# Optimization experiments

Hardware: AMD Instinct MI355X
Metric: run time of the kernel (lower is better)

## Reference

```python
import jax, jax.numpy as jnp
import numpy as np

B, S, D = 2, 2048, 1024
H = 16
HD = D // H  # 64


def setup_inputs() -> dict:
    key = jax.random.key(0)
    ks = jax.random.split(key, 6)
    x = jax.random.normal(ks[0], (B, S, D), dtype=jnp.float32)
    sc = 1.0 / np.sqrt(D)
    Wq = jax.random.normal(ks[1], (D, D), dtype=jnp.float32) * sc
    Wk = jax.random.normal(ks[2], (D, D), dtype=jnp.float32) * sc
    Wv = jax.random.normal(ks[3], (D, D), dtype=jnp.float32) * sc
    Wo = jax.random.normal(ks[4], (D, D), dtype=jnp.float32) * sc
    bo = jax.random.normal(ks[5], (D,), dtype=jnp.float32) * 0.01
    return {"x": x, "Wq": Wq, "Wk": Wk, "Wv": Wv, "Wo": Wo, "bo": bo}


def reference(x, Wq, Wk, Wv, Wo, bo):
    b, s, d = x.shape
    # projections (torch Linear: y = x @ W.T; weights here stored as [d_in, d_out])
    Q = (x @ Wq).reshape(b, s, H, HD).transpose(0, 2, 1, 3)  # [b,h,s,hd]
    K = (x @ Wk).reshape(b, s, H, HD).transpose(0, 2, 1, 3)
    V = (x @ Wv).reshape(b, s, H, HD).transpose(0, 2, 1, 3)
    scores = jnp.einsum("bhqd,bhkd->bhqk", Q, K) / np.sqrt(HD)
    causal = jnp.triu(jnp.ones((s, s), dtype=bool), k=1)  # True above diagonal
    scores = jnp.where(causal[None, None], -jnp.inf, scores)
    attn = jax.nn.softmax(scores, axis=-1)
    # dropout_rate = 0.0 -> identity (eval-mode reference)
    ctx = jnp.einsum("bhqk,bhkd->bhqd", attn, V)
    ctx = ctx.transpose(0, 2, 1, 3).reshape(b, s, d)
    return ctx @ Wo + bo
```

## Files before the change

kernel.cpp:

```cpp
#include <hip/hip_runtime.h>
#include <hip/hip_bf16.h>

#define B_  2
#define S_  2048
#define D_  1024
#define H_  16
#define HD_ 64
#define M_  (B_*S_)

typedef __attribute__((ext_vector_type(8))) short short8;
typedef __attribute__((ext_vector_type(4))) float f32x4;

#define MFMA16(a, b, c) __builtin_amdgcn_mfma_f32_16x16x32_bf16((a), (b), (c), 0, 0, 0)

static __device__ inline short f2bf(float f) {
    union { float f; unsigned u; } v; v.f = f;
    unsigned r = v.u + 0x7FFFu + ((v.u >> 16) & 1u);
    return (short)(r >> 16);
}

static __device__ __forceinline__ float fexp2(float x) {
    float r;
    asm volatile("v_exp_f32 %0, %1\n\ts_nop 1" : "=v"(r) : "v"(x));
    return r;
}

static __device__ __forceinline__ unsigned cvt_pk_bf16(float lo, float hi) {
    unsigned r;
    asm volatile("v_cvt_pk_bf16_f32 %0, %1, %2" : "=v"(r) : "v"(lo), "v"(hi));
    return r;
}

static __device__ __forceinline__ void gl_lds16(const short* g, short* l) {
    __builtin_amdgcn_global_load_lds(
        (const __attribute__((address_space(1))) void*)g,
        (__attribute__((address_space(3))) void*)l, 16, 0, 0);
}

__global__ void cvt_x_kernel(const float* __restrict__ x, short* __restrict__ xb, int n4) {
    int i = blockIdx.x * blockDim.x + threadIdx.x;
    int stride = gridDim.x * blockDim.x;
    for (; i < n4; i += stride) {
        float4 v = ((const float4*)x)[i];
        short4 o;
        o.x = f2bf(v.x); o.y = f2bf(v.y); o.z = f2bf(v.z); o.w = f2bf(v.w);
        ((short4*)xb)[i] = o;
    }
}

__global__ void transpose_w4_kernel(const float* __restrict__ Wq, const float* __restrict__ Wk,
                                    const float* __restrict__ Wv, const float* __restrict__ Wo,
                                    short* __restrict__ Wqkvt, short* __restrict__ Wot) {
    __shared__ float tile[32][33];
    int z = blockIdx.z;
    const float* W = (z == 0) ? Wq : (z == 1) ? Wk : (z == 2) ? Wv : Wo;
    short* Wt = (z == 3) ? Wot : (Wqkvt + ((size_t)z << 20));
    int tx = threadIdx.x & 31, ty = threadIdx.x >> 5;
    int n0 = blockIdx.x * 32, k0 = blockIdx.y * 32;
#pragma unroll
    for (int i = 0; i < 4; ++i)
        tile[ty + 8 * i][tx] = W[(size_t)(k0 + ty + 8 * i) * D_ + n0 + tx];
    __syncthreads();
#pragma unroll
    for (int i = 0; i < 4; ++i)
        Wt[(size_t)(n0 + ty + 8 * i) * D_ + k0 + tx] = f2bf(tile[tx][ty + 8 * i]);
}

__global__ void reduce_bias_kernel(float* __restrict__ out, const float* __restrict__ p1,
                                   const float* __restrict__ bias, int n4) {
    int i = blockIdx.x * blockDim.x + threadIdx.x;
    int stride = gridDim.x * blockDim.x;
    for (; i < n4; i += stride) {
        float4 a = ((const float4*)out)[i];
        float4 b = ((const float4*)p1)[i];
        float4 c = ((const float4*)bias)[i & 255];
        a.x += b.x + c.x; a.y += b.y + c.y; a.z += b.z + c.z; a.w += b.w + c.w;
        ((float4*)out)[i] = a;
    }
}

__global__ __launch_bounds__(512) void gemm_qkv(const short* __restrict__ A,
                                                const short* __restrict__ Bt,
                                                short* __restrict__ out) {
    __shared__ __align__(16) short Asm[2][128 * 32];
    __shared__ __align__(16) short Bsm[2][256 * 32];
    int wg = (blockIdx.x & 7) * 48 + (blockIdx.x >> 3);
    int bn = wg >> 5, bm = wg & 31;
    int tid = threadIdx.x, l = tid & 63, w = tid >> 6;
    int lhi = l >> 4, llo = l & 15;
    int wm = w >> 2, wn = w & 3;

    f32x4 acc[4][4];
#pragma unroll
    for (int m = 0; m < 4; ++m)
#pragma unroll
        for (int n = 0; n < 4; ++n) acc[m][n] = (f32x4){0.f, 0.f, 0.f, 0.f};

    const short* Ag = A + (size_t)(bm * 128) * 1024;
    const short* Bg = Bt + (size_t)(bn * 256) * 1024;
    int ca = tid;
    int ra = ((ca >> 5) << 3) | (ca & 7), sa = ((ca >> 3) & 3) ^ (ra & 3);
    int cb0 = tid, cb1 = tid + 512;
    int rb0 = ((cb0 >> 5) << 3) | (cb0 & 7), sb0 = ((cb0 >> 3) & 3) ^ (rb0 & 3);
    int rb1 = ((cb1 >> 5) << 3) | (cb1 & 7), sb1 = ((cb1 >> 3) & 3) ^ (rb1 & 3);

    auto stage = [&](int buf, int k0) {
        gl_lds16(Ag + (size_t)ra * 1024 + k0 + sa * 8, &Asm[buf][ca * 8]);
        gl_lds16(Bg + (size_t)rb0 * 1024 + k0 + sb0 * 8, &Bsm[buf][cb0 * 8]);
        gl_lds16(Bg + (size_t)rb1 * 1024 + k0 + sb1 * 8, &Bsm[buf][cb1 * 8]);
    };

    int cia[4], cib[4];
#pragma unroll
    for (int m = 0; m < 4; ++m) {
        int row = wm * 64 + m * 16 + llo;
        cia[m] = ((row >> 3) << 5) | (((lhi ^ row) & 3) << 3) | (row & 7);
    }
#pragma unroll
    for (int n = 0; n < 4; ++n) {
        int row = wn * 64 + n * 16 + llo;
        cib[n] = ((row >> 3) << 5) | (((lhi ^ row) & 3) << 3) | (row & 7);
    }

    stage(0, 0);
    for (int i = 0; i < 32; ++i) {
        asm volatile("s_waitcnt vmcnt(0)" ::: "memory");
        __builtin_amdgcn_s_barrier();
        asm volatile("" ::: "memory");
        if (i + 1 < 32) stage((i + 1) & 1, (i + 1) * 32);
        int cur = i & 1;
        short8 af[4], bf[4];
#pragma unroll
        for (int m = 0; m < 4; ++m) af[m] = *(const short8*)&Asm[cur][cia[m] * 8];
#pragma unroll
        for (int n = 0; n < 4; ++n) bf[n] = *(const short8*)&Bsm[cur][cib[n] * 8];
#pragma unroll
        for (int m = 0; m < 4; ++m)
#pragma unroll
            for (int n = 0; n < 4; ++n)
                acc[m][n] = MFMA16(af[m], bf[n], acc[m][n]);
    }

    int rowb = bm * 128 + wm * 64, colb = bn * 256 + wn * 64;
#pragma unroll
    for (int m = 0; m < 4; ++m) {
#pragma unroll
        for (int n = 0; n < 4; ++n) {
            int col = colb + n * 16 + llo;
#pragma unroll
            for (int j = 0; j < 4; ++j) {
                int row = rowb + m * 16 + lhi * 4 + j;
                float v = acc[m][n][j];
                int proj = col >> 10, n1 = col & 1023;
                int h = n1 >> 6, hd = n1 & 63;
                int b = row >> 11, s = row & 2047;
                size_t off;
                if (proj == 0)
                    off = ((size_t)(b * 16 + h) * 2048 + s) * 64 + hd;
                else if (proj == 1)
                    off = (size_t)M_ * D_ + ((size_t)(b * 16 + h) * 2048 + s) * 64 + hd;
                else
                    off = (size_t)2 * M_ * D_ + ((size_t)(b * 16 + h) * 64 + hd) * 2048 + s;
                out[off] = f2bf(v);
            }
        }
    }
}

__global__ __launch_bounds__(256) void gemm_out(const short* __restrict__ A,
                                                const short* __restrict__ Bt,
                                                float* __restrict__ pscr,
                                                float* __restrict__ out) {
    __shared__ __align__(16) short Asm[2][128 * 32];
    __shared__ __align__(16) short Bsm[2][128 * 32];
    int X = blockIdx.x & 7, t = blockIdx.x >> 3;
    int ks = t & 1, bm = t >> 1, bn = X;
    int tid = threadIdx.x, l = tid & 63, w = tid >> 6;
    int lhi = l >> 4, llo = l & 15;
    int wm = w >> 1, wn = w & 1;

    f32x4 acc[4][4];
#pragma unroll
    for (int m = 0; m < 4; ++m)
#pragma unroll
        for (int n = 0; n < 4; ++n) acc[m][n] = (f32x4){0.f, 0.f, 0.f, 0.f};

    const short* Ag = A + (size_t)(bm * 128) * 1024 + ks * 512;
    const short* Bg = Bt + (size_t)(bn * 128) * 1024 + ks * 512;
    int c0 = tid, c1 = 256 + tid;
    int r0 = ((c0 >> 5) << 3) | (c0 & 7), s0 = ((c0 >> 3) & 3) ^ (r0 & 3);
    int r1 = ((c1 >> 5) << 3) | (c1 & 7), s1 = ((c1 >> 3) & 3) ^ (r1 & 3);

    auto stage = [&](int buf, int k0) {
        gl_lds16(Ag + (size_t)r0 * 1024 + k0 + s0 * 8, &Asm[buf][c0 * 8]);
        gl_lds16(Ag + (size_t)r1 * 1024 + k0 + s1 * 8, &Asm[buf][c1 * 8]);
        gl_lds16(Bg + (size_t)r0 * 1024 + k0 + s0 * 8, &Bsm[buf][c0 * 8]);
        gl_lds16(Bg + (size_t)r1 * 1024 + k0 + s1 * 8, &Bsm[buf][c1 * 8]);
    };

    int cia[4], cib[4];
#pragma unroll
    for (int m = 0; m < 4; ++m) {
        int row = wm * 64 + m * 16 + llo;
        cia[m] = ((row >> 3) << 5) | (((lhi ^ row) & 3) << 3) | (row & 7);
    }
#pragma unroll
    for (int n = 0; n < 4; ++n) {
        int row = wn * 64 + n * 16 + llo;
        cib[n] = ((row >> 3) << 5) | (((lhi ^ row) & 3) << 3) | (row & 7);
    }

    stage(0, 0);
    for (int i = 0; i < 16; ++i) {
        asm volatile("s_waitcnt vmcnt(0)" ::: "memory");
        __builtin_amdgcn_s_barrier();
        asm volatile("" ::: "memory");
        if (i + 1 < 16) stage((i + 1) & 1, (i + 1) * 32);
        int cur = i & 1;
        short8 af[4], bf[4];
#pragma unroll
        for (int m = 0; m < 4; ++m) af[m] = *(const short8*)&Asm[cur][cia[m] * 8];
#pragma unroll
        for (int n = 0; n < 4; ++n) bf[n] = *(const short8*)&Bsm[cur][cib[n] * 8];
#pragma unroll
        for (int m = 0; m < 4; ++m)
#pragma unroll
            for (int n = 0; n < 4; ++n)
                acc[m][n] = MFMA16(af[m], bf[n], acc[m][n]);
    }

    float* o = ks ? pscr : out;
    int rowb = bm * 128 + wm * 64, colb = bn * 128 + wn * 64;
#pragma unroll
    for (int m = 0; m < 4; ++m)
#pragma unroll
        for (int n = 0; n < 4; ++n) {
            int col = colb + n * 16 + llo;
#pragma unroll
            for (int j = 0; j < 4; ++j) {
                int row = rowb + m * 16 + lhi * 4 + j;
                o[(size_t)row * 1024 + col] = acc[m][n][j];
            }
        }
}

__global__ __launch_bounds__(512) void attn_kernel(const short* __restrict__ Q,
                                                   const short* __restrict__ Kg,
                                                   const short* __restrict__ Vt,
                                                   short* __restrict__ ctx) {
    __shared__ __align__(16) char kvbuf[2][16384];
    __shared__ __align__(16) char plds[8][2048];
    int tid = threadIdx.x, w = tid >> 6, l = tid & 63;
    int lhi = l >> 4, llo = l & 15;
    int bh = blockIdx.x & 31, qp = blockIdx.x >> 5;
    int b = bh >> 4, h = bh & 15;
    char* pb = plds[w];

    const short* Qh = Q + (size_t)bh * S_ * HD_;
    const short* Kh = Kg + (size_t)bh * S_ * HD_;
    const short* Vh = Vt + (size_t)bh * HD_ * S_;

    int qbA = qp, qbB = 15 - qp;
    int NTA = 2 * qp + 2;
    const int NT = 34;

    int srow = tid >> 3;
    int ssrc = (16 * (tid & 7)) ^ ((srow & 7) << 4);
    auto stage = [&](char* buf, int c0) {
        gl_lds16(Kh + (size_t)(c0 + srow) * HD_ + (ssrc >> 1), (short*)(buf + tid * 16));
        gl_lds16(Vh + (size_t)srow * S_ + c0 + (ssrc >> 1), (short*)(buf + 8192 + tid * 16));
    };

    f32x4 O[4];
#pragma unroll
    for (int n = 0; n < 4; ++n) O[n] = (f32x4){0.f, 0.f, 0.f, 0.f};
    float lpart[4] = {0.f, 0.f, 0.f, 0.f};

    auto writeOut = [&](int qb) {
        int qbs = qb * 128 + w * 16;
#pragma unroll
        for (int j = 0; j < 4; ++j) {
            float ls = lpart[j];
            ls += __shfl_xor(ls, 1);
            ls += __shfl_xor(ls, 2);
            ls += __shfl_xor(ls, 4);
            ls += __shfl_xor(ls, 8);
            float inv = 1.0f / ls;
            int row = qbs + lhi * 4 + j;
            size_t base = ((size_t)(b * S_ + row)) * D_ + h * HD_;
#pragma unroll
            for (int n = 0; n < 4; ++n)
                ctx[base + n * 16 + llo] = f2bf(O[n][j] * inv);
        }
    };

    const float SC = 0.18033688f;
    const float M2 = 17.312340f;

    int qbase = qbA * 128 + w * 16;
    short8 aq0 = *(const short8*)(Qh + (size_t)(qbase + llo) * HD_ + 8 * lhi);
    short8 aq1 = *(const short8*)(Qh + (size_t)(qbase + llo) * HD_ + 32 + 8 * lhi);

    stage(kvbuf[0], 0);

    for (int i = 0; i < NT; ++i) {
        asm volatile("s_waitcnt vmcnt(0)" ::: "memory");
        __builtin_amdgcn_s_barrier();
        asm volatile("" ::: "memory");
        int kt = (i < NTA) ? i : i - NTA;
        int c0 = kt * 64;
        if (i + 1 < NT) {
            int ni = i + 1;
            int nkt = (ni < NTA) ? ni : ni - NTA;
            stage(kvbuf[ni & 1], nkt * 64);
        }
        const char* kb = kvbuf[i & 1];
        const char* vb = kb + 8192;

        if (c0 <= qbase + 15) {
            f32x4 sc4[4];
#pragma unroll
            for (int cb = 0; cb < 4; ++cb) {
                int row = cb * 16 + llo;
                int sw = (row & 7) << 4;
                short8 kf0 = *(const short8*)(kb + row * 128 + ((16 * lhi) ^ sw));
                short8 kf1 = *(const short8*)(kb + row * 128 + ((64 + 16 * lhi) ^ sw));
                f32x4 z = (f32x4){0.f, 0.f, 0.f, 0.f};
                z = MFMA16(aq0, kf0, z);
                z = MFMA16(aq1, kf1, z);
                sc4[cb] = z;
            }
            bool diag = (c0 + 63 > qbase);
#pragma unroll
            for (int j = 0; j < 4; ++j) {
                int qr = qbase + lhi * 4 + j;
                float v0 = fmaf(sc4[0][j], SC, -M2);
                float v1 = fmaf(sc4[1][j], SC, -M2);
                float v2 = fmaf(sc4[2][j], SC, -M2);
                float v3 = fmaf(sc4[3][j], SC, -M2);
                if (diag) {
                    if (c0 + llo > qr)      v0 = -1e30f;
                    if (c0 + 16 + llo > qr) v1 = -1e30f;
                    if (c0 + 32 + llo > qr) v2 = -1e30f;
                    if (c0 + 48 + llo > qr) v3 = -1e30f;
                }
                float p0 = fexp2(v0), p1 = fexp2(v1);
                float p2 = fexp2(v2), p3 = fexp2(v3);
                lpart[j] += (p0 + p1) + (p2 + p3);
                unsigned pk01 = cvt_pk_bf16(p0, p1);
                unsigned pk23 = cvt_pk_bf16(p2, p3);
                int r = lhi * 4 + j;
                char* rb = pb + r * 128;
                int sw = (r & 7) << 4;
                *(short*)(rb + ((2 * llo) ^ sw))      = (short)(pk01);
                *(short*)(rb + ((2 * llo + 32) ^ sw)) = (short)(pk01 >> 16);
                *(short*)(rb + ((2 * llo + 64) ^ sw)) = (short)(pk23);
                *(short*)(rb + ((2 * llo + 96) ^ sw)) = (short)(pk23 >> 16);
            }
            int swr = (llo & 7) << 4;
            short8 pa0 = *(const short8*)(pb + llo * 128 + ((16 * lhi) ^ swr));
            short8 pa1 = *(const short8*)(pb + llo * 128 + ((64 + 16 * lhi) ^ swr));
#pragma unroll
            for (int n = 0; n < 4; ++n) {
                int row = n * 16 + llo;
                int sw = (row & 7) << 4;
                short8 vf0 = *(const short8*)(vb + row * 128 + ((16 * lhi) ^ sw));
                short8 vf1 = *(const short8*)(vb + row * 128 + ((64 + 16 * lhi) ^ sw));
                O[n] = MFMA16(pa0, vf0, O[n]);
                O[n] = MFMA16(pa1, vf1, O[n]);
            }
        }

        if (i == NTA - 1) {
            writeOut(qbA);
#pragma unroll
            for (int n = 0; n < 4; ++n) O[n] = (f32x4){0.f, 0.f, 0.f, 0.f};
            lpart[0] = lpart[1] = lpart[2] = lpart[3] = 0.f;
            qbase = qbB * 128 + w * 16;
            aq0 = *(const short8*)(Qh + (size_t)(qbase + llo) * HD_ + 8 * lhi);
            aq1 = *(const short8*)(Qh + (size_t)(qbase + llo) * HD_ + 32 + 8 * lhi);
        }
    }
    writeOut(qbB);
}

extern "C" void kernel_launch(void* const* d_in, const int* in_sizes, int n_in,
                              void* d_out, int out_size, void* d_ws, size_t ws_size,
                              hipStream_t stream) {
    const float* x  = (const float*)d_in[0];
    const float* Wq = (const float*)d_in[1];
    const float* Wk = (const float*)d_in[2];
    const float* Wv = (const float*)d_in[3];
    const float* Wo = (const float*)d_in[4];
    const float* bo = (const float*)d_in[5];
    float* out = (float*)d_out;

    char* ws = (char*)d_ws;
    short* xb    = (short*)(ws);
    short* Wqkvt = (short*)(ws + (size_t)(8 << 20));
    short* Wot   = (short*)(ws + (size_t)(14 << 20));
    short* Qb    = (short*)(ws + (size_t)(16 << 20));
    short* Kb    = Qb + (size_t)M_ * D_;
    short* Vtb   = Qb + (size_t)2 * M_ * D_;
    short* ctx   = xb;
    float* pscr  = (float*)(ws + (size_t)(16 << 20));

    cvt_x_kernel<<<2048, 256, 0, stream>>>(x, xb, M_ * D_ / 4);
    transpose_w4_kernel<<<dim3(32, 32, 4), 256, 0, stream>>>(Wq, Wk, Wv, Wo, Wqkvt, Wot);

    gemm_qkv<<<384, 512, 0, stream>>>(xb, Wqkvt, Qb);
    attn_kernel<<<256, 512, 0, stream>>>(Qb, Kb, Vtb, ctx);
    gemm_out<<<512, 256, 0, stream>>>(ctx, Wot, pscr, out);
    reduce_bias_kernel<<<2048, 256, 0, stream>>>(out, pscr, bo, M_ * D_ / 4);
}
```

Before: 145.0 us.

## Fuse prep kernels, drop split-K output GEMM with bias epilogue, retile QKV GEMM

Merges the x conversion and the weight transposes into one prep launch. The QKV GEMM is retiled from 128x256 tiles with 512 threads to 128x128 tiles with 256 threads, giving 768 blocks instead of 384. The output GEMM drops split-K and the separate reduce+bias kernel, using 64x128 tiles over the full K and adding the bias in the epilogue. This removes two launches and a scratch-buffer round trip, at the cost of less per-block reuse in both GEMMs and a longer K loop in gemm_out.

```diff
diff --git a/kernel.cpp b/kernel.cpp
--- a/kernel.cpp
+++ b/kernel.cpp
@@ -37,22 +37,26 @@
         (__attribute__((address_space(3))) void*)l, 16, 0, 0);
 }
 
-__global__ void cvt_x_kernel(const float* __restrict__ x, short* __restrict__ xb, int n4) {
-    int i = blockIdx.x * blockDim.x + threadIdx.x;
-    int stride = gridDim.x * blockDim.x;
-    for (; i < n4; i += stride) {
-        float4 v = ((const float4*)x)[i];
-        short4 o;
-        o.x = f2bf(v.x); o.y = f2bf(v.y); o.z = f2bf(v.z); o.w = f2bf(v.w);
-        ((short4*)xb)[i] = o;
-    }
-}
-
-__global__ void transpose_w4_kernel(const float* __restrict__ Wq, const float* __restrict__ Wk,
-                                    const float* __restrict__ Wv, const float* __restrict__ Wo,
-                                    short* __restrict__ Wqkvt, short* __restrict__ Wot) {
+__global__ void prep_kernel(const float* __restrict__ x,
+                            const float* __restrict__ Wq, const float* __restrict__ Wk,
+                            const float* __restrict__ Wv, const float* __restrict__ Wo,
+                            short* __restrict__ xb,
+                            short* __restrict__ Wqkvt, short* __restrict__ Wot) {
+    int z = blockIdx.z;
+    if (z == 4) {
+        int bid = blockIdx.y * 32 + blockIdx.x;
+        int base = bid * 1024 + threadIdx.x;
+#pragma unroll
+        for (int it = 0; it < 4; ++it) {
+            int i = base + it * 256;
+            float4 v = ((const float4*)x)[i];
+            short4 o;
+            o.x = f2bf(v.x); o.y = f2bf(v.y); o.z = f2bf(v.z); o.w = f2bf(v.w);
+            ((short4*)xb)[i] = o;
+        }
+        return;
+    }
     __shared__ float tile[32][33];
-    int z = blockIdx.z;
     const float* W = (z == 0) ? Wq : (z == 1) ? Wk : (z == 2) ? Wv : Wo;
     short* Wt = (z == 3) ? Wot : (Wqkvt + ((size_t)z << 20));
     int tx = threadIdx.x & 31, ty = threadIdx.x >> 5;
@@ -66,29 +70,17 @@
         Wt[(size_t)(n0 + ty + 8 * i) * D_ + k0 + tx] = f2bf(tile[tx][ty + 8 * i]);
 }
 
-__global__ void reduce_bias_kernel(float* __restrict__ out, const float* __restrict__ p1,
-                                   const float* __restrict__ bias, int n4) {
-    int i = blockIdx.x * blockDim.x + threadIdx.x;
-    int stride = gridDim.x * blockDim.x;
-    for (; i < n4; i += stride) {
-        float4 a = ((const float4*)out)[i];
-        float4 b = ((const float4*)p1)[i];
-        float4 c = ((const float4*)bias)[i & 255];
-        a.x += b.x + c.x; a.y += b.y + c.y; a.z += b.z + c.z; a.w += b.w + c.w;
-        ((float4*)out)[i] = a;
-    }
-}
-
-__global__ __launch_bounds__(512) void gemm_qkv(const short* __restrict__ A,
+__global__ __launch_bounds__(256) void gemm_qkv(const short* __restrict__ A,
                                                 const short* __restrict__ Bt,
                                                 short* __restrict__ out) {
     __shared__ __align__(16) short Asm[2][128 * 32];
-    __shared__ __align__(16) short Bsm[2][256 * 32];
-    int wg = (blockIdx.x & 7) * 48 + (blockIdx.x >> 3);
-    int bn = wg >> 5, bm = wg & 31;
+    __shared__ __align__(16) short Bsm[2][128 * 32];
+    const int NBX = 3;
+    int X = blockIdx.x & 7, t = blockIdx.x >> 3;
+    int bm = t / NBX, bn = X * NBX + t % NBX;
     int tid = threadIdx.x, l = tid & 63, w = tid >> 6;
     int lhi = l >> 4, llo = l & 15;
-    int wm = w >> 2, wn = w & 3;
+    int wm = w >> 1, wn = w & 1;
 
     f32x4 acc[4][4];
 #pragma unroll
@@ -97,17 +89,16 @@
         for (int n = 0; n < 4; ++n) acc[m][n] = (f32x4){0.f, 0.f, 0.f, 0.f};
 
     const short* Ag = A + (size_t)(bm * 128) * 1024;
-    const short* Bg = Bt + (size_t)(bn * 256) * 1024;
-    int ca = tid;
-    int ra = ((ca >> 5) << 3) | (ca & 7), sa = ((ca >> 3) & 3) ^ (ra & 3);
-    int cb0 = tid, cb1 = tid + 512;
-    int rb0 = ((cb0 >> 5) << 3) | (cb0 & 7), sb0 = ((cb0 >> 3) & 3) ^ (rb0 & 3);
-    int rb1 = ((cb1 >> 5) << 3) | (cb1 & 7), sb1 = ((cb1 >> 3) & 3) ^ (rb1 & 3);
+    const short* Bg = Bt + (size_t)(bn * 128) * 1024;
+    int c0 = tid, c1 = 256 + tid;
+    int r0 = ((c0 >> 5) << 3) | (c0 & 7), s0 = ((c0 >> 3) & 3) ^ (r0 & 3);
+    int r1 = ((c1 >> 5) << 3) | (c1 & 7), s1 = ((c1 >> 3) & 3) ^ (r1 & 3);
 
     auto stage = [&](int buf, int k0) {
-        gl_lds16(Ag + (size_t)ra * 1024 + k0 + sa * 8, &Asm[buf][ca * 8]);
-        gl_lds16(Bg + (size_t)rb0 * 1024 + k0 + sb0 * 8, &Bsm[buf][cb0 * 8]);
-        gl_lds16(Bg + (size_t)rb1 * 1024 + k0 + sb1 * 8, &Bsm[buf][cb1 * 8]);
+        gl_lds16(Ag + (size_t)r0 * 1024 + k0 + s0 * 8, &Asm[buf][c0 * 8]);
+        gl_lds16(Ag + (size_t)r1 * 1024 + k0 + s1 * 8, &Asm[buf][c1 * 8]);
+        gl_lds16(Bg + (size_t)r0 * 1024 + k0 + s0 * 8, &Bsm[buf][c0 * 8]);
+        gl_lds16(Bg + (size_t)r1 * 1024 + k0 + s1 * 8, &Bsm[buf][c1 * 8]);
     };
 
     int cia[4], cib[4];
@@ -141,7 +132,7 @@
                 acc[m][n] = MFMA16(af[m], bf[n], acc[m][n]);
     }
 
-    int rowb = bm * 128 + wm * 64, colb = bn * 256 + wn * 64;
+    int rowb = bm * 128 + wm * 64, colb = bn * 128 + wn * 64;
 #pragma unroll
     for (int m = 0; m < 4; ++m) {
 #pragma unroll
@@ -167,79 +158,77 @@
     }
 }
 
-__global__ __launch_bounds__(256) void gemm_out(const short* __restrict__ A,
-                                                const short* __restrict__ Bt,
-                                                float* __restrict__ pscr,
-                                                float* __restrict__ out) {
-    __shared__ __align__(16) short Asm[2][128 * 32];
+__global__ __launch_bounds__(256, 6) void gemm_out(const short* __restrict__ A,
+                                                   const short* __restrict__ Bt,
+                                                   const float* __restrict__ bias,
+                                                   float* __restrict__ out) {
+    __shared__ __align__(16) short Asm[2][64 * 32];
     __shared__ __align__(16) short Bsm[2][128 * 32];
-    int X = blockIdx.x & 7, t = blockIdx.x >> 3;
-    int ks = t & 1, bm = t >> 1, bn = X;
+    int bn = blockIdx.x & 7, bm = blockIdx.x >> 3;
     int tid = threadIdx.x, l = tid & 63, w = tid >> 6;
     int lhi = l >> 4, llo = l & 15;
-    int wm = w >> 1, wn = w & 1;
-
-    f32x4 acc[4][4];
+
+    f32x4 acc[4][2];
 #pragma unroll
     for (int m = 0; m < 4; ++m)
 #pragma unroll
-        for (int n = 0; n < 4; ++n) acc[m][n] = (f32x4){0.f, 0.f, 0.f, 0.f};
-
-    const short* Ag = A + (size_t)(bm * 128) * 1024 + ks * 512;
-    const short* Bg = Bt + (size_t)(bn * 128) * 1024 + ks * 512;
-    int c0 = tid, c1 = 256 + tid;
-    int r0 = ((c0 >> 5) << 3) | (c0 & 7), s0 = ((c0 >> 3) & 3) ^ (r0 & 3);
-    int r1 = ((c1 >> 5) << 3) | (c1 & 7), s1 = ((c1 >> 3) & 3) ^ (r1 & 3);
+        for (int n = 0; n < 2; ++n) acc[m][n] = (f32x4){0.f, 0.f, 0.f, 0.f};
+
+    const short* Ag = A + (size_t)(bm * 64) * 1024;
+    const short* Bg = Bt + (size_t)(bn * 128) * 1024;
+    int ca = tid;
+    int ra = ((ca >> 5) << 3) | (ca & 7), sa = ((ca >> 3) & 3) ^ (ra & 3);
+    int cb0 = tid, cb1 = tid + 256;
+    int rb0 = ((cb0 >> 5) << 3) | (cb0 & 7), sb0 = ((cb0 >> 3) & 3) ^ (rb0 & 3);
+    int rb1 = ((cb1 >> 5) << 3) | (cb1 & 7), sb1 = ((cb1 >> 3) & 3) ^ (rb1 & 3);
 
     auto stage = [&](int buf, int k0) {
-        gl_lds16(Ag + (size_t)r0 * 1024 + k0 + s0 * 8, &Asm[buf][c0 * 8]);
-        gl_lds16(Ag + (size_t)r1 * 1024 + k0 + s1 * 8, &Asm[buf][c1 * 8]);
-        gl_lds16(Bg + (size_t)r0 * 1024 + k0 + s0 * 8, &Bsm[buf][c0 * 8]);
-        gl_lds16(Bg + (size_t)r1 * 1024 + k0 + s1 * 8, &Bsm[buf][c1 * 8]);
+        gl_lds16(Ag + (size_t)ra * 1024 + k0 + sa * 8, &Asm[buf][ca * 8]);
+        gl_lds16(Bg + (size_t)rb0 * 1024 + k0 + sb0 * 8, &Bsm[buf][cb0 * 8]);
+        gl_lds16(Bg + (size_t)rb1 * 1024 + k0 + sb1 * 8, &Bsm[buf][cb1 * 8]);
     };
 
-    int cia[4], cib[4];
+    int cia[4], cib[2];
 #pragma unroll
     for (int m = 0; m < 4; ++m) {
-        int row = wm * 64 + m * 16 + llo;
+        int row = m * 16 + llo;
         cia[m] = ((row >> 3) << 5) | (((lhi ^ row) & 3) << 3) | (row & 7);
     }
 #pragma unroll
-    for (int n = 0; n < 4; ++n) {
-        int row = wn * 64 + n * 16 + llo;
+    for (int n = 0; n < 2; ++n) {
+        int row = w * 32 + n * 16 + llo;
         cib[n] = ((row >> 3) << 5) | (((lhi ^ row) & 3) << 3) | (row & 7);
     }
 
     stage(0, 0);
-    for (int i = 0; i < 16; ++i) {
+    for (int i = 0; i < 32; ++i) {
         asm volatile("s_waitcnt vmcnt(0)" ::: "memory");
         __builtin_amdgcn_s_barrier();
         asm volatile("" ::: "memory");
-        if (i + 1 < 16) stage((i + 1) & 1, (i + 1) * 32);
+        if (i + 1 < 32) stage((i + 1) & 1, (i + 1) * 32);
         int cur = i & 1;
-        short8 af[4], bf[4];
+        short8 af[4], bf[2];
 #pragma unroll
         for (int m = 0; m < 4; ++m) af[m] = *(const short8*)&Asm[cur][cia[m] * 8];
 #pragma unroll
-        for (int n = 0; n < 4; ++n) bf[n] = *(const short8*)&Bsm[cur][cib[n] * 8];
+        for (int n = 0; n < 2; ++n) bf[n] = *(const short8*)&Bsm[cur][cib[n] * 8];
 #pragma unroll
         for (int m = 0; m < 4; ++m)
 #pragma unroll
-            for (int n = 0; n < 4; ++n)
+            for (int n = 0; n < 2; ++n)
                 acc[m][n] = MFMA16(af[m], bf[n], acc[m][n]);
     }
 
-    float* o = ks ? pscr : out;
-    int rowb = bm * 128 + wm * 64, colb = bn * 128 + wn * 64;
+    int rowb = bm * 64, colb = bn * 128 + w * 32;
 #pragma unroll
     for (int m = 0; m < 4; ++m)
 #pragma unroll
-        for (int n = 0; n < 4; ++n) {
+        for (int n = 0; n < 2; ++n) {
             int col = colb + n * 16 + llo;
 #pragma unroll
             for (int j = 0; j < 4; ++j) {
                 int row = rowb + m * 16 + lhi * 4 + j;
-                o[(size_t)row * 1024 + col] = acc[m][n][j];
+                out[(size_t)row * 1024 + col] = acc[m][n][j] + bias[col];
             }
         }
 }
@@ -403,13 +392,9 @@
     short* Kb    = Qb + (size_t)M_ * D_;
     short* Vtb   = Qb + (size_t)2 * M_ * D_;
     short* ctx   = xb;
-    float* pscr  = (float*)(ws + (size_t)(16 << 20));
-
-    cvt_x_kernel<<<2048, 256, 0, stream>>>(x, xb, M_ * D_ / 4);
-    transpose_w4_kernel<<<dim3(32, 32, 4), 256, 0, stream>>>(Wq, Wk, Wv, Wo, Wqkvt, Wot);
-
-    gemm_qkv<<<384, 512, 0, stream>>>(xb, Wqkvt, Qb);
+
+    prep_kernel<<<dim3(32, 32, 5), 256, 0, stream>>>(x, Wq, Wk, Wv, Wo, xb, Wqkvt, Wot);
+    gemm_qkv<<<768, 256, 0, stream>>>(xb, Wqkvt, Qb);
     attn_kernel<<<256, 512, 0, stream>>>(Qb, Kb, Vtb, ctx);
-    gemm_out<<<512, 256, 0, stream>>>(ctx, Wot, pscr, out);
-    reduce_bias_kernel<<<2048, 256, 0, stream>>>(out, pscr, bo, M_ * D_ / 4);
-}
+    gemm_out<<<512, 256, 0, stream>>>(ctx, Wot, bo, out);
+}
```

Result: faster. 133.8 us (-7.7%).
